# Optimization experiments

Measured on AMD Instinct MI355X. Metric: run time of the kernel, lower is better.

Reference implementation:

```python
import jax, jax.numpy as jnp
import numpy as np
import math

N_HIDDEN = 1024
ATT_DIM = 16   # number of heads; per-head q/k dim is 1 (see split()/transpose in source)
B, L = 2, 1024


def setup_inputs() -> dict:
    key = jax.random.key(0)
    ks = jax.random.split(key, 8)
    s = 1.0 / math.sqrt(N_HIDDEN)
    return {
        "x": jax.random.normal(ks[0], (B, L, N_HIDDEN), jnp.float32),
        "mask": jnp.zeros((B, L), jnp.float32),  # 0 = keep (scores *= 1 - mask)
        "Wq": jax.random.normal(ks[1], (N_HIDDEN, ATT_DIM), jnp.float32) * s,
        "bq": jnp.zeros((ATT_DIM,), jnp.float32),
        "Wk": jax.random.normal(ks[2], (N_HIDDEN, ATT_DIM), jnp.float32) * s,
        "bk": jnp.zeros((ATT_DIM,), jnp.float32),
        "Wv": jax.random.normal(ks[3], (N_HIDDEN, N_HIDDEN), jnp.float32) * s,
        "bv": jnp.zeros((N_HIDDEN,), jnp.float32),
        "ln_g": jnp.ones((N_HIDDEN,), jnp.float32),
        "ln_b": jnp.zeros((N_HIDDEN,), jnp.float32),
        # zero_factor is nn.Parameter(zeros(1)) in source; use small random so output != x
        "zero_factor": jax.random.normal(ks[4], (1,), jnp.float32) * 0.1,
        "angle": jax.random.normal(ks[5], (1, ATT_DIM, 1, 1, 1), jnp.float32),
    }


def _layernorm(x, g, b, eps=1e-5):
    mu = jnp.mean(x, axis=-1, keepdims=True)
    var = jnp.var(x, axis=-1, keepdims=True)
    return (x - mu) * jax.lax.rsqrt(var + eps) * g + b


def reference(x, mask, Wq, bq, Wk, bk, Wv, bv, ln_g, ln_b, zero_factor, angle):
    b, l, d = x.shape
    h = ATT_DIM
    xn = _layernorm(x, ln_g, ln_b)
    q = xn @ Wq + bq                      # [b,l,h]
    k = xn @ Wk + bk                      # [b,l,h]
    v = xn @ Wv + bv                      # [b,l,d]
    q = jnp.transpose(q, (0, 2, 1))[..., None]          # [b,h,l,1]
    k = jnp.transpose(k, (0, 2, 1))[..., None]          # [b,h,l,1]
    v = v.reshape(b, l, h, d // h).transpose(0, 2, 1, 3)  # [b,h,l,d/h]

    q_ = q[:, :, :, None, :]              # [b,h,l,1,1]
    k_ = k[:, :, None, :, :]              # [b,h,1,l,1]
    ca, sa = jnp.cos(angle), jnp.sin(angle)  # [1,h,1,1,1]
    # complex rotation e^{i*angle} * (q + i k), broadcast pairwise -> [b,h,l,l,1]
    real = ca * q_ - sa * k_
    imag = sa * q_ + ca * k_
    # softmax over the (real, imag) pair (stable, single max/sub)
    m = jnp.maximum(real, imag)
    er = jnp.exp(real - m)
    ei = jnp.exp(imag - m)
    comp = (er * real + ei * imag) / (er + ei)   # gated composite component
    scores = jax.nn.softplus(comp)[..., 0]       # pairwise softplus score [b,h,l,l]
    scores = scores * (1.0 - mask[:, None, None, :])
    scores = scores * (math.sqrt(2.0) / math.sqrt(l))
    ctx = jax.nn.gelu(scores @ v, approximate=False)     # [b,h,l,d/h]
    out = x + ctx.transpose(0, 2, 1, 3).reshape(b, l, d) * zero_factor
    return out
```

## Files before the change

### kernel.cpp

```cpp
#include <hip/hip_runtime.h>
#include <hip/hip_bf16.h>
#include <math.h>

#define NH 1024
#define SEQ 1024
#define BATCH 2
#define NHEAD 16
#define DHEAD 64

typedef __attribute__((ext_vector_type(8))) short short8;
typedef __attribute__((ext_vector_type(4))) float f32x4;
typedef __attribute__((ext_vector_type(2))) float f32x2;

__device__ __forceinline__ unsigned short f2bf(float f) {
    unsigned u = __builtin_bit_cast(unsigned, f);
    unsigned r = 0x7FFFu + ((u >> 16) & 1u);
    u += r;
    return (unsigned short)(u >> 16);
}
__device__ __forceinline__ unsigned pk_bf2(float lo, float hi) {
    return (unsigned)f2bf(lo) | ((unsigned)f2bf(hi) << 16);
}
__device__ __forceinline__ unsigned cvtpk_bf16(float lo, float hi) {
    unsigned r;
    asm("v_cvt_pk_bf16_f32 %0, %1, %2" : "=v"(r) : "v"(lo), "v"(hi));
    return r;
}

typedef __attribute__((address_space(1))) const unsigned int as1_uint;
typedef __attribute__((address_space(3))) unsigned int as3_uint;
__device__ __forceinline__ void gload16(const void* g, void* l) {
    __builtin_amdgcn_global_load_lds((as1_uint*)g, (as3_uint*)l, 16, 0, 0);
}

__global__ __launch_bounds__(256) void k_pre(
    const float* __restrict__ x, const float* __restrict__ ln_g,
    const float* __restrict__ ln_b, const float* __restrict__ Wv,
    const float* __restrict__ Wq, const float* __restrict__ Wk,
    const float* __restrict__ mask,
    unsigned short* __restrict__ xnb, unsigned short* __restrict__ WvT,
    unsigned short* __restrict__ WqkT, float* __restrict__ maskf)
{
    __shared__ __align__(16) unsigned char smem[16704];
    int bid = blockIdx.x;
    int t = threadIdx.x;

    if (bid < BATCH * SEQ / 4) {
        int w = t >> 6, lane = t & 63;
        int row = bid * 4 + w;
        float4 xv[4];
#pragma unroll
        for (int c = 0; c < 4; ++c)
            xv[c] = *(const float4*)(x + (size_t)row * NH + c * 256 + lane * 4);
        float s = 0.f, ss = 0.f;
#pragma unroll
        for (int c = 0; c < 4; ++c) {
            s  += xv[c].x + xv[c].y + xv[c].z + xv[c].w;
            ss += xv[c].x*xv[c].x + xv[c].y*xv[c].y + xv[c].z*xv[c].z + xv[c].w*xv[c].w;
        }
#pragma unroll
        for (int off = 32; off > 0; off >>= 1) {
            s  += __shfl_xor(s, off);
            ss += __shfl_xor(ss, off);
        }
        float mu  = s * (1.0f / NH);
        float var = ss * (1.0f / NH) - mu * mu;
        float rstd = rsqrtf(var + 1e-5f);
#pragma unroll
        for (int c = 0; c < 4; ++c) {
            float4 gv = *(const float4*)(ln_g + c * 256 + lane * 4);
            float4 bv2 = *(const float4*)(ln_b + c * 256 + lane * 4);
            float o0 = (xv[c].x - mu) * rstd * gv.x + bv2.x;
            float o1 = (xv[c].y - mu) * rstd * gv.y + bv2.y;
            float o2 = (xv[c].z - mu) * rstd * gv.z + bv2.z;
            float o3 = (xv[c].w - mu) * rstd * gv.w + bv2.w;
            uint2 u;
            u.x = pk_bf2(o0, o1);
            u.y = pk_bf2(o2, o3);
            *(uint2*)(xnb + (size_t)row * NH + c * 256 + lane * 4) = u;
        }
        return;
    }
    int u = bid - BATCH * SEQ / 4;
    if (u < 256) {
        float (*T)[65] = (float(*)[65])smem;
        int k0 = (u >> 4) * 64, n0 = (u & 15) * 64;
        int row = t >> 2, c4 = t & 3;
#pragma unroll
        for (int s = 0; s < 4; ++s) {
            float4 v = *(const float4*)(Wv + (size_t)(k0 + row) * NH + n0 + c4 * 16 + s * 4);
            *(float4*)&T[row][c4 * 16 + s * 4] = v;
        }
        __syncthreads();
        unsigned short tmp[16] __attribute__((aligned(16)));
#pragma unroll
        for (int s = 0; s < 16; ++s) tmp[s] = f2bf(T[c4 * 16 + s][row]);
        unsigned short* dst = WvT + (size_t)(n0 + row) * NH + k0 + c4 * 16;
        *(short8*)dst = *(const short8*)&tmp[0];
        *(short8*)(dst + 8) = *(const short8*)&tmp[8];
    } else if (u < 512) {
        int i = (u - 256) * 256 + t;
        int n = i >> 10, k = i & 1023;
        float v = (n < 16) ? Wq[k * 16 + n] : (n < 32 ? Wk[k * 16 + (n - 16)] : 0.0f);
        WqkT[i] = f2bf(v);
    } else {
        int i = (u - 512) * 256 + t;
        maskf[i] = (1.0f - mask[i]) * 0.044194173824159216f * 0.69314718055994531f;
    }
}

__global__ __launch_bounds__(256) void k_gemm(
    const unsigned short* __restrict__ xnb,
    const unsigned short* __restrict__ WvT, const unsigned short* __restrict__ WqkT,
    const float* __restrict__ bv, const float* __restrict__ bq, const float* __restrict__ bk,
    const float* __restrict__ angle,
    unsigned short* __restrict__ vt, float* __restrict__ qT, float* __restrict__ kT,
    float* __restrict__ Ek)
{
    __shared__ unsigned short lds[2][8192];
    int t = threadIdx.x, w = t >> 6, lane = t & 63, g = lane >> 4, r = lane & 15;
    int bid = blockIdx.x;
    int lb = (bid & 7) * 68 + (bid >> 3);
    int nt_ = lb % 17, mt = lb / 17;
    int i0 = mt * 64, n0 = nt_ * 64;
    const unsigned short* Bsrc = (nt_ < 16) ? (WvT + (size_t)n0 * NH) : WqkT;

    f32x4 acc[2][2];
#pragma unroll
    for (int a = 0; a < 2; ++a)
#pragma unroll
        for (int c = 0; c < 2; ++c) acc[a][c] = (f32x4)(0.0f);

    auto stage = [&](int buf, int k0) {
#pragma unroll
        for (int i = 0; i < 2; ++i) {
            int o = i * 4096 + w * 1024 + lane * 16;
            int rr = o >> 7, cb = o & 127;
            int sc = (cb ^ ((rr & 7) << 4)) >> 1;
            gload16(xnb + (size_t)(i0 + rr) * NH + k0 + sc, &lds[buf][o >> 1]);
        }
#pragma unroll
        for (int i = 0; i < 2; ++i) {
            int o = i * 4096 + w * 1024 + lane * 16;
            int rr = o >> 7, cb = o & 127;
            int sc = (cb ^ ((rr & 7) << 4)) >> 1;
            gload16(Bsrc + (size_t)rr * NH + k0 + sc, &lds[buf][4096 + (o >> 1)]);
        }
    };

    int mbase = (w >> 1) * 32, nbase = (w & 1) * 32;
    int swz = (r & 7) << 4;

    auto compute = [&](int buf) {
        const unsigned short* As = lds[buf];
        const unsigned short* Bs = lds[buf] + 4096;
#pragma unroll
        for (int ks = 0; ks < 2; ++ks) {
            int kbyte = ks * 64 + g * 16;
            int kb = kbyte ^ swz;
            short8 af[2], bfm[2];
#pragma unroll
            for (int mf = 0; mf < 2; ++mf) {
                int row = mbase + mf * 16 + r;
                af[mf] = *(const short8*)(As + ((row * 128 + kb) >> 1));
            }
#pragma unroll
            for (int nf = 0; nf < 2; ++nf) {
                int rowB = nbase + nf * 16 + r;
                bfm[nf] = *(const short8*)(Bs + ((rowB * 128 + kb) >> 1));
            }
#pragma unroll
            for (int mf = 0; mf < 2; ++mf)
#pragma unroll
                for (int nf = 0; nf < 2; ++nf)
                    acc[mf][nf] = __builtin_amdgcn_mfma_f32_16x16x32_bf16(af[mf], bfm[nf], acc[mf][nf], 0, 0, 0);
        }
    };

    stage(0, 0);
    stage(1, 64);
    asm volatile("s_waitcnt vmcnt(4)" ::: "memory");
    __builtin_amdgcn_sched_barrier(0);
    __builtin_amdgcn_s_barrier();
    int cur = 0;
#pragma unroll 1
    for (int kt = 0; kt < 14; ++kt) {
        compute(cur);
        asm volatile("s_waitcnt lgkmcnt(0)" ::: "memory");
        __builtin_amdgcn_sched_barrier(0);
        __builtin_amdgcn_s_barrier();
        stage(cur, (kt + 2) * 64);
        asm volatile("s_waitcnt vmcnt(4)" ::: "memory");
        __builtin_amdgcn_sched_barrier(0);
        __builtin_amdgcn_s_barrier();
        cur ^= 1;
    }
    compute(cur);
    asm volatile("s_waitcnt lgkmcnt(0)" ::: "memory");
    __builtin_amdgcn_sched_barrier(0);
    __builtin_amdgcn_s_barrier();
    asm volatile("s_waitcnt vmcnt(0)" ::: "memory");
    __builtin_amdgcn_sched_barrier(0);
    __builtin_amdgcn_s_barrier();
    compute(cur ^ 1);

    if (nt_ < 16) {
        unsigned short (*tsm)[72] = (unsigned short(*)[72])&lds[0][0];
        __syncthreads();
#pragma unroll
        for (int nf = 0; nf < 2; ++nf) {
            float bvv = bv[n0 + nbase + nf * 16 + r];
#pragma unroll
            for (int mf = 0; mf < 2; ++mf)
#pragma unroll
                for (int j = 0; j < 4; ++j)
                    tsm[nbase + nf * 16 + r][mbase + mf * 16 + g * 4 + j] = f2bf(acc[mf][nf][j] + bvv);
        }
        __syncthreads();
        int b = mt >> 4;
        int jc0 = (mt & 15) * 64;
        int d = t >> 2, jb = (t & 3) * 16;
        unsigned short* dst = vt + ((size_t)((b * 16 + nt_) * 64 + d)) * 1024 + jc0 + jb;
        *(short8*)dst = *(const short8*)&tsm[d][jb];
        *(short8*)(dst + 8) = *(const short8*)&tsm[d][jb + 8];
    } else {
        const float L2E = 1.4426950408889634f;
#pragma unroll
        for (int nf = 0; nf < 2; ++nf) {
            int n = nbase + nf * 16 + r;
            if (n < 32) {
                float bb = (n < 16) ? bq[n] : bk[n - 16];
                float* dstp = (n < 16) ? (qT + n * 2048) : (kT + (n - 16) * 2048);
                bool isk = (n >= 16);
                float c2 = 0.0f;
                if (isk) {
                    float ang = angle[n - 16];
                    c2 = cosf(ang) + sinf(ang);
                }
#pragma unroll
                for (int mf = 0; mf < 2; ++mf)
#pragma unroll
                    for (int j = 0; j < 4; ++j) {
                        int gi = i0 + mbase + mf * 16 + g * 4 + j;
                        float val = acc[mf][nf][j] + bb;
                        dstp[gi] = val;
                        if (isk)
                            Ek[(n - 16) * 2048 + gi] = __builtin_amdgcn_exp2f(c2 * val * L2E);
                    }
            }
        }
    }
}

__global__ __launch_bounds__(256, 4) void k_attn(
    const float* __restrict__ qT, const float* __restrict__ kT,
    const float* __restrict__ Ek,
    const unsigned short* __restrict__ vt, const float* __restrict__ x,
    const float* __restrict__ maskf, const float* __restrict__ angle,
    const float* __restrict__ zfp, float* __restrict__ out)
{
    __shared__ __align__(16) unsigned char smem[30720];
    float* tbl = (float*)smem;
    float (*red)[3][32][20] = (float(*)[3][32][20])smem;

    int bid = blockIdx.x;
    int lb = (bid & 7) * 128 + (bid >> 3);
    int qt = lb & 31;
    int h = (lb >> 5) & 15;
    int b = lb >> 9;
    int t = threadIdx.x;
    int w = t >> 6, lane = t & 63, g = lane >> 4, r = lane & 15;
    int i0 = qt * 32;

    const float L2E = 1.4426950408889634f;
    float ang = angle[h];
    float cs = cosf(ang), sn = sinf(ang);
    float c1L = (cs - sn) * L2E, snL = sn * L2E;
    float nc2L = -(cs + sn) * L2E, csL = cs * L2E;
    float zf = zfp[0];

    const float* qcol = qT + h * 2048 + b * 1024;
    const float* kcol = kT + h * 2048 + b * 1024;
    const float* ecol = Ek + h * 2048 + b * 1024;
    const float* mrow = maskf + b * 1024;
    const unsigned short* vhead = vt + ((size_t)(b * 16 + h)) * 64 * 1024;

    int jbase = w * 256 + g * 8;

    short8 bfr[2][4];
#pragma unroll
    for (int nb = 0; nb < 4; ++nb)
        bfr[0][nb] = *(const short8*)(vhead + (size_t)(nb * 16 + r) * 1024 + jbase);

    {
        float4 a = *(const float4*)(kcol + t * 4);
        float4 m4 = *(const float4*)(mrow + t * 4);
        float4 e4 = *(const float4*)(ecol + t * 4);
        *(float4*)&tbl[t * 4] = a;
        *(float4*)&tbl[1024 + t * 4] = m4;
        *(float4*)&tbl[2048 + t * 4] = e4;
    }

    float qv0 = qcol[i0 + r];
    float qv1 = qcol[i0 + 16 + r];
    f32x2 c1qL = {c1L * qv0, c1L * qv1};
    f32x2 snqL = {snL * qv0, snL * qv1};
    f32x2 Eu = {__builtin_amdgcn_exp2f(-c1qL.x), __builtin_amdgcn_exp2f(-c1qL.y)};

    f32x4 acc[2][4];
#pragma unroll
    for (int m = 0; m < 2; ++m)
#pragma unroll
        for (int nb = 0; nb < 4; ++nb) acc[m][nb] = (f32x4)(0.0f);

    __syncthreads();

#pragma unroll 2
    for (int it = 0; it < 8; ++it) {
        int cur = it & 1, nxt = cur ^ 1;
        int j = jbase + it * 32;
        float4 kva = *(const float4*)&tbl[j];
        float4 kvb = *(const float4*)&tbl[j + 4];
        float4 ffa = *(const float4*)&tbl[1024 + j];
        float4 ffb = *(const float4*)&tbl[1024 + j + 4];
        float4 eea = *(const float4*)&tbl[2048 + j];
        float4 eeb = *(const float4*)&tbl[2048 + j + 4];
        if (it < 7) {
            int jn = j + 32;
#pragma unroll
            for (int nb = 0; nb < 4; ++nb)
                bfr[nxt][nb] = *(const short8*)(vhead + (size_t)(nb * 16 + r) * 1024 + jn);
        }
        float kk[8] = {kva.x, kva.y, kva.z, kva.w, kvb.x, kvb.y, kvb.z, kvb.w};
        float ff[8] = {ffa.x, ffa.y, ffa.z, ffa.w, ffb.x, ffb.y, ffb.z, ffb.w};
        float ee_[8] = {eea.x, eea.y, eea.z, eea.w, eeb.x, eeb.y, eeb.z, eeb.w};

        unsigned a0[4], a1[4];
#pragma unroll
        for (int p = 0; p < 4; ++p) {
            float sa[2], sb[2];
#pragma unroll
            for (int q2 = 0; q2 < 2; ++q2) {
                float kv = kk[p * 2 + q2];
                float f  = ff[p * 2 + q2];
                float E  = ee_[p * 2 + q2];
                float naL = nc2L * kv;
                float ikL = csL * kv;
                f32x2 ddL = c1qL + naL;
                f32x2 imL = snqL + ikL;
                f32x2 P  = Eu * E;
                f32x2 den = P + 1.0f;
                f32x2 sg  = {__builtin_amdgcn_rcpf(den.x), __builtin_amdgcn_rcpf(den.y)};
                f32x2 compL = __builtin_elementwise_fma(ddL, sg, imL);
                f32x2 ee2 = {__builtin_amdgcn_exp2f(compL.x), __builtin_amdgcn_exp2f(compL.y)};
                f32x2 vv = ee2 + 1.0f;
                f32x2 lg = {__builtin_amdgcn_logf(vv.x), __builtin_amdgcn_logf(vv.y)};
                f32x2 s2 = lg * f;
                sa[q2] = s2.x;
                sb[q2] = s2.y;
            }
            a0[p] = cvtpk_bf16(sa[0], sa[1]);
            a1[p] = cvtpk_bf16(sb[0], sb[1]);
        }
        unsigned av0[4] = {a0[0], a0[1], a0[2], a0[3]};
        unsigned av1[4] = {a1[0], a1[1], a1[2], a1[3]};
        short8 af0 = *(short8*)av0;
        short8 af1 = *(short8*)av1;

        __builtin_amdgcn_s_setprio(1);
#pragma unroll
        for (int nb = 0; nb < 4; ++nb) {
            acc[0][nb] = __builtin_amdgcn_mfma_f32_16x16x32_bf16(af0, bfr[cur][nb], acc[0][nb], 0, 0, 0);
            acc[1][nb] = __builtin_amdgcn_mfma_f32_16x16x32_bf16(af1, bfr[cur][nb], acc[1][nb], 0, 0, 0);
        }
        __builtin_amdgcn_s_setprio(0);
    }

    __syncthreads();

#pragma unroll
    for (int nb = 0; nb < 4; ++nb) {
        if (nb != w) {
            int idx = w - (w > nb ? 1 : 0);
#pragma unroll
            for (int m = 0; m < 2; ++m)
#pragma unroll
                for (int jj = 0; jj < 4; ++jj)
                    red[nb][idx][m * 16 + g * 4 + jj][r] = acc[m][nb][jj];
        }
    }
    __syncthreads();

#pragma unroll
    for (int m = 0; m < 2; ++m)
#pragma unroll
        for (int jj = 0; jj < 4; ++jj) {
            int lrow = m * 16 + g * 4 + jj;
            float c = acc[m][w][jj] + red[w][0][lrow][r]
                                    + red[w][1][lrow][r]
                                    + red[w][2][lrow][r];
            float gl = 0.5f * c * (1.0f + erff(c * 0.70710678118654752f));
            size_t base = ((size_t)(b * 1024 + i0 + lrow)) * 1024 + h * 64 + w * 16 + r;
            out[base] = x[base] + gl * zf;
        }
}

extern "C" void kernel_launch(void* const* d_in, const int* in_sizes, int n_in,
                              void* d_out, int out_size, void* d_ws, size_t ws_size,
                              hipStream_t stream) {
    const float* x      = (const float*)d_in[0];
    const float* mask   = (const float*)d_in[1];
    const float* Wq     = (const float*)d_in[2];
    const float* bq     = (const float*)d_in[3];
    const float* Wk     = (const float*)d_in[4];
    const float* bk     = (const float*)d_in[5];
    const float* Wv     = (const float*)d_in[6];
    const float* bv     = (const float*)d_in[7];
    const float* ln_g   = (const float*)d_in[8];
    const float* ln_b   = (const float*)d_in[9];
    const float* zf     = (const float*)d_in[10];
    const float* angle  = (const float*)d_in[11];
    float* out = (float*)d_out;

    unsigned short* xnb  = (unsigned short*)d_ws;
    unsigned short* vt   = xnb + 2097152;
    unsigned short* WvT  = vt + 2097152;
    unsigned short* WqkT = WvT + 1048576;
    float* qT    = (float*)(WqkT + 65536);
    float* kT    = qT + 32768;
    float* maskf = kT + 32768;
    float* Ek    = maskf + 2048;

    k_pre<<<BATCH * SEQ / 4 + 520, 256, 0, stream>>>(x, ln_g, ln_b, Wv, Wq, Wk, mask,
                                                     xnb, WvT, WqkT, maskf);
    k_gemm<<<544, 256, 0, stream>>>(xnb, WvT, WqkT, bv, bq, bk, angle, vt, qT, kT, Ek);
    k_attn<<<1024, 256, 0, stream>>>(qT, kT, Ek, vt, x, maskf, angle, zf, out);
}
```

Before: 48.04 us.

## Fold mask and key coefficients into GEMM epilogue, halve GEMM M-tile

The key/value GEMM now uses 32-row M tiles, launching twice as many blocks for better occupancy across CUs. The mask-and-scale factor moves from the attention inner loop into V before bf16 conversion, so scores are no longer multiplied per element. The GEMM also precomputes the per-key rotation terms (Ak, Bk), which removes two multiplies per score in the hot attention loop. The cost is extra global writes and reads for Ak/Bk, less reuse per GEMM tile, and a slight bf16 rounding change from scaling V instead of the scores.

```diff
diff --git a/kernel.cpp b/kernel.cpp
--- a/kernel.cpp
+++ b/kernel.cpp
@@ -113,73 +113,68 @@
     const unsigned short* __restrict__ xnb,
     const unsigned short* __restrict__ WvT, const unsigned short* __restrict__ WqkT,
     const float* __restrict__ bv, const float* __restrict__ bq, const float* __restrict__ bk,
-    const float* __restrict__ angle,
-    unsigned short* __restrict__ vt, float* __restrict__ qT, float* __restrict__ kT,
-    float* __restrict__ Ek)
+    const float* __restrict__ angle, const float* __restrict__ maskf,
+    unsigned short* __restrict__ vt, float* __restrict__ qT,
+    float* __restrict__ Ak, float* __restrict__ Bk, float* __restrict__ Ek)
 {
-    __shared__ unsigned short lds[2][8192];
+    __shared__ unsigned short lds[2][6144];
     int t = threadIdx.x, w = t >> 6, lane = t & 63, g = lane >> 4, r = lane & 15;
     int bid = blockIdx.x;
-    int lb = (bid & 7) * 68 + (bid >> 3);
+    int lb = (bid & 7) * 136 + (bid >> 3);
     int nt_ = lb % 17, mt = lb / 17;
-    int i0 = mt * 64, n0 = nt_ * 64;
+    int i0 = mt * 32, n0 = nt_ * 64;
     const unsigned short* Bsrc = (nt_ < 16) ? (WvT + (size_t)n0 * NH) : WqkT;
 
-    f32x4 acc[2][2];
-#pragma unroll
-    for (int a = 0; a < 2; ++a)
-#pragma unroll
-        for (int c = 0; c < 2; ++c) acc[a][c] = (f32x4)(0.0f);
+    f32x4 acc[2];
+    acc[0] = (f32x4)(0.0f);
+    acc[1] = (f32x4)(0.0f);
 
     auto stage = [&](int buf, int k0) {
+        {
+            int o = w * 1024 + lane * 16;
+            int rr = o >> 7, cb = o & 127;
+            int sc = (cb ^ ((rr & 7) << 4)) >> 1;
+            gload16(xnb + (size_t)(i0 + rr) * NH + k0 + sc, &lds[buf][o >> 1]);
+        }
 #pragma unroll
         for (int i = 0; i < 2; ++i) {
             int o = i * 4096 + w * 1024 + lane * 16;
             int rr = o >> 7, cb = o & 127;
             int sc = (cb ^ ((rr & 7) << 4)) >> 1;
-            gload16(xnb + (size_t)(i0 + rr) * NH + k0 + sc, &lds[buf][o >> 1]);
-        }
-#pragma unroll
-        for (int i = 0; i < 2; ++i) {
-            int o = i * 4096 + w * 1024 + lane * 16;
-            int rr = o >> 7, cb = o & 127;
-            int sc = (cb ^ ((rr & 7) << 4)) >> 1;
-            gload16(Bsrc + (size_t)rr * NH + k0 + sc, &lds[buf][4096 + (o >> 1)]);
+            gload16(Bsrc + (size_t)rr * NH + k0 + sc, &lds[buf][2048 + (o >> 1)]);
         }
     };
 
-    int mbase = (w >> 1) * 32, nbase = (w & 1) * 32;
+    int mbase = (w >> 1) * 16, nbase = (w & 1) * 32;
     int swz = (r & 7) << 4;
 
     auto compute = [&](int buf) {
         const unsigned short* As = lds[buf];
-        const unsigned short* Bs = lds[buf] + 4096;
+        const unsigned short* Bs = lds[buf] + 2048;
 #pragma unroll
         for (int ks = 0; ks < 2; ++ks) {
             int kbyte = ks * 64 + g * 16;
             int kb = kbyte ^ swz;
-            short8 af[2], bfm[2];
-#pragma unroll
-            for (int mf = 0; mf < 2; ++mf) {
-                int row = mbase + mf * 16 + r;
-                af[mf] = *(const short8*)(As + ((row * 128 + kb) >> 1));
+            short8 af;
+            {
+                int row = mbase + r;
+                af = *(const short8*)(As + ((row * 128 + kb) >> 1));
             }
+            short8 bfm[2];
 #pragma unroll
             for (int nf = 0; nf < 2; ++nf) {
                 int rowB = nbase + nf * 16 + r;
                 bfm[nf] = *(const short8*)(Bs + ((rowB * 128 + kb) >> 1));
             }
 #pragma unroll
-            for (int mf = 0; mf < 2; ++mf)
-#pragma unroll
-                for (int nf = 0; nf < 2; ++nf)
-                    acc[mf][nf] = __builtin_amdgcn_mfma_f32_16x16x32_bf16(af[mf], bfm[nf], acc[mf][nf], 0, 0, 0);
+            for (int nf = 0; nf < 2; ++nf)
+                acc[nf] = __builtin_amdgcn_mfma_f32_16x16x32_bf16(af, bfm[nf], acc[nf], 0, 0, 0);
         }
     };
 
     stage(0, 0);
     stage(1, 64);
-    asm volatile("s_waitcnt vmcnt(4)" ::: "memory");
+    asm volatile("s_waitcnt vmcnt(3)" ::: "memory");
     __builtin_amdgcn_sched_barrier(0);
     __builtin_amdgcn_s_barrier();
     int cur = 0;
@@ -190,7 +185,7 @@
         __builtin_amdgcn_sched_barrier(0);
         __builtin_amdgcn_s_barrier();
         stage(cur, (kt + 2) * 64);
-        asm volatile("s_waitcnt vmcnt(4)" ::: "memory");
+        asm volatile("s_waitcnt vmcnt(3)" ::: "memory");
         __builtin_amdgcn_sched_barrier(0);
         __builtin_amdgcn_s_barrier();
         cur ^= 1;
@@ -205,59 +200,60 @@
     compute(cur ^ 1);
 
     if (nt_ < 16) {
-        unsigned short (*tsm)[72] = (unsigned short(*)[72])&lds[0][0];
+        unsigned short (*tsm)[40] = (unsigned short(*)[40])&lds[0][0];
         __syncthreads();
+        float4 mrow4 = *(const float4*)(maskf + i0 + mbase + g * 4);
+        const float* mr = (const float*)&mrow4;
 #pragma unroll
         for (int nf = 0; nf < 2; ++nf) {
             float bvv = bv[n0 + nbase + nf * 16 + r];
 #pragma unroll
-            for (int mf = 0; mf < 2; ++mf)
-#pragma unroll
-                for (int j = 0; j < 4; ++j)
-                    tsm[nbase + nf * 16 + r][mbase + mf * 16 + g * 4 + j] = f2bf(acc[mf][nf][j] + bvv);
+            for (int j = 0; j < 4; ++j)
+                tsm[nbase + nf * 16 + r][mbase + g * 4 + j] = f2bf((acc[nf][j] + bvv) * mr[j]);
         }
         __syncthreads();
-        int b = mt >> 4;
-        int jc0 = (mt & 15) * 64;
-        int d = t >> 2, jb = (t & 3) * 16;
+        int b = mt >> 5;
+        int jc0 = (mt & 31) * 32;
+        int d = t >> 2, jb = (t & 3) * 8;
         unsigned short* dst = vt + ((size_t)((b * 16 + nt_) * 64 + d)) * 1024 + jc0 + jb;
         *(short8*)dst = *(const short8*)&tsm[d][jb];
-        *(short8*)(dst + 8) = *(const short8*)&tsm[d][jb + 8];
     } else {
         const float L2E = 1.4426950408889634f;
 #pragma unroll
         for (int nf = 0; nf < 2; ++nf) {
             int n = nbase + nf * 16 + r;
-            if (n < 32) {
-                float bb = (n < 16) ? bq[n] : bk[n - 16];
-                float* dstp = (n < 16) ? (qT + n * 2048) : (kT + (n - 16) * 2048);
-                bool isk = (n >= 16);
-                float c2 = 0.0f;
-                if (isk) {
-                    float ang = angle[n - 16];
-                    c2 = cosf(ang) + sinf(ang);
+            if (n < 16) {
+                float bb2 = bq[n];
+#pragma unroll
+                for (int j = 0; j < 4; ++j)
+                    qT[n * 2048 + i0 + mbase + g * 4 + j] = acc[nf][j] + bb2;
+            } else if (n < 32) {
+                int h = n - 16;
+                float bb2 = bk[h];
+                float ang = angle[h];
+                float csv = cosf(ang), snv = sinf(ang);
+                float c2 = csv + snv;
+#pragma unroll
+                for (int j = 0; j < 4; ++j) {
+                    int gi = i0 + mbase + g * 4 + j;
+                    float val = acc[nf][j] + bb2;
+                    float c2L = c2 * val * L2E;
+                    Ak[h * 2048 + gi] = -c2L;
+                    Bk[h * 2048 + gi] = csv * val * L2E;
+                    Ek[h * 2048 + gi] = __builtin_amdgcn_exp2f(c2L);
                 }
-#pragma unroll
-                for (int mf = 0; mf < 2; ++mf)
-#pragma unroll
-                    for (int j = 0; j < 4; ++j) {
-                        int gi = i0 + mbase + mf * 16 + g * 4 + j;
-                        float val = acc[mf][nf][j] + bb;
-                        dstp[gi] = val;
-                        if (isk)
-                            Ek[(n - 16) * 2048 + gi] = __builtin_amdgcn_exp2f(c2 * val * L2E);
-                    }
             }
         }
     }
 }
 
 __global__ __launch_bounds__(256, 4) void k_attn(
-    const float* __restrict__ qT, const float* __restrict__ kT,
+    const float* __restrict__ qT,
+    const float* __restrict__ Ak, const float* __restrict__ Bk,
     const float* __restrict__ Ek,
     const unsigned short* __restrict__ vt, const float* __restrict__ x,
-    const float* __restrict__ maskf, const float* __restrict__ angle,
-    const float* __restrict__ zfp, float* __restrict__ out)
+    const float* __restrict__ angle, const float* __restrict__ zfp,
+    float* __restrict__ out)
 {
     __shared__ __align__(16) unsigned char smem[30720];
     float* tbl = (float*)smem;
@@ -276,13 +272,12 @@
     float ang = angle[h];
     float cs = cosf(ang), sn = sinf(ang);
     float c1L = (cs - sn) * L2E, snL = sn * L2E;
-    float nc2L = -(cs + sn) * L2E, csL = cs * L2E;
     float zf = zfp[0];
 
     const float* qcol = qT + h * 2048 + b * 1024;
-    const float* kcol = kT + h * 2048 + b * 1024;
+    const float* acol = Ak + h * 2048 + b * 1024;
+    const float* bcol = Bk + h * 2048 + b * 1024;
     const float* ecol = Ek + h * 2048 + b * 1024;
-    const float* mrow = maskf + b * 1024;
     const unsigned short* vhead = vt + ((size_t)(b * 16 + h)) * 64 * 1024;
 
     int jbase = w * 256 + g * 8;
@@ -293,11 +288,11 @@
         bfr[0][nb] = *(const short8*)(vhead + (size_t)(nb * 16 + r) * 1024 + jbase);
 
     {
-        float4 a = *(const float4*)(kcol + t * 4);
-        float4 m4 = *(const float4*)(mrow + t * 4);
+        float4 a = *(const float4*)(acol + t * 4);
+        float4 b4 = *(const float4*)(bcol + t * 4);
         float4 e4 = *(const float4*)(ecol + t * 4);
         *(float4*)&tbl[t * 4] = a;
-        *(float4*)&tbl[1024 + t * 4] = m4;
+        *(float4*)&tbl[1024 + t * 4] = b4;
         *(float4*)&tbl[2048 + t * 4] = e4;
     }
 
@@ -319,10 +314,10 @@
     for (int it = 0; it < 8; ++it) {
         int cur = it & 1, nxt = cur ^ 1;
         int j = jbase + it * 32;
-        float4 kva = *(const float4*)&tbl[j];
-        float4 kvb = *(const float4*)&tbl[j + 4];
-        float4 ffa = *(const float4*)&tbl[1024 + j];
-        float4 ffb = *(const float4*)&tbl[1024 + j + 4];
+        float4 aka = *(const float4*)&tbl[j];
+        float4 akb = *(const float4*)&tbl[j + 4];
+        float4 bka = *(const float4*)&tbl[1024 + j];
+        float4 bkb = *(const float4*)&tbl[1024 + j + 4];
         float4 eea = *(const float4*)&tbl[2048 + j];
         float4 eeb = *(const float4*)&tbl[2048 + j + 4];
         if (it < 7) {
@@ -331,8 +326,8 @@
             for (int nb = 0; nb < 4; ++nb)
                 bfr[nxt][nb] = *(const short8*)(vhead + (size_t)(nb * 16 + r) * 1024 + jn);
         }
-        float kk[8] = {kva.x, kva.y, kva.z, kva.w, kvb.x, kvb.y, kvb.z, kvb.w};
-        float ff[8] = {ffa.x, ffa.y, ffa.z, ffa.w, ffb.x, ffb.y, ffb.z, ffb.w};
+        float aa[8] = {aka.x, aka.y, aka.z, aka.w, akb.x, akb.y, akb.z, akb.w};
+        float bb_[8] = {bka.x, bka.y, bka.z, bka.w, bkb.x, bkb.y, bkb.z, bkb.w};
         float ee_[8] = {eea.x, eea.y, eea.z, eea.w, eeb.x, eeb.y, eeb.z, eeb.w};
 
         unsigned a0[4], a1[4];
@@ -341,13 +336,11 @@
             float sa[2], sb[2];
 #pragma unroll
             for (int q2 = 0; q2 < 2; ++q2) {
-                float kv = kk[p * 2 + q2];
-                float f  = ff[p * 2 + q2];
+                float a_ = aa[p * 2 + q2];
+                float b_ = bb_[p * 2 + q2];
                 float E  = ee_[p * 2 + q2];
-                float naL = nc2L * kv;
-                float ikL = csL * kv;
-                f32x2 ddL = c1qL + naL;
-                f32x2 imL = snqL + ikL;
+                f32x2 ddL = c1qL + a_;
+                f32x2 imL = snqL + b_;
                 f32x2 P  = Eu * E;
                 f32x2 den = P + 1.0f;
                 f32x2 sg  = {__builtin_amdgcn_rcpf(den.x), __builtin_amdgcn_rcpf(den.y)};
@@ -355,9 +348,8 @@
                 f32x2 ee2 = {__builtin_amdgcn_exp2f(compL.x), __builtin_amdgcn_exp2f(compL.y)};
                 f32x2 vv = ee2 + 1.0f;
                 f32x2 lg = {__builtin_amdgcn_logf(vv.x), __builtin_amdgcn_logf(vv.y)};
-                f32x2 s2 = lg * f;
-                sa[q2] = s2.x;
-                sb[q2] = s2.y;
+                sa[q2] = lg.x;
+                sb[q2] = lg.y;
             }
             a0[p] = cvtpk_bf16(sa[0], sa[1]);
             a1[p] = cvtpk_bf16(sb[0], sb[1]);
@@ -427,12 +419,14 @@
     unsigned short* WvT  = vt + 2097152;
     unsigned short* WqkT = WvT + 1048576;
     float* qT    = (float*)(WqkT + 65536);
-    float* kT    = qT + 32768;
-    float* maskf = kT + 32768;
-    float* Ek    = maskf + 2048;
+    float* Ak    = qT + 32768;
+    float* Bk    = Ak + 32768;
+    float* Ek    = Bk + 32768;
+    float* maskf = Ek + 32768;
 
     k_pre<<<BATCH * SEQ / 4 + 520, 256, 0, stream>>>(x, ln_g, ln_b, Wv, Wq, Wk, mask,
                                                      xnb, WvT, WqkT, maskf);
-    k_gemm<<<544, 256, 0, stream>>>(xnb, WvT, WqkT, bv, bq, bk, angle, vt, qT, kT, Ek);
-    k_attn<<<1024, 256, 0, stream>>>(qT, kT, Ek, vt, x, maskf, angle, zf, out);
-}
+    k_gemm<<<64 * 17, 256, 0, stream>>>(xnb, WvT, WqkT, bv, bq, bk, angle, maskf,
+                                        vt, qT, Ak, Bk, Ek);
+    k_attn<<<1024, 256, 0, stream>>>(qT, Ak, Bk, Ek, vt, x, angle, zf, out);
+}
```

Result: slower. 49.12 us (+2.2%).
